# Kernel optimization log

Hardware: AMD Instinct MI355X
Metric: run time of the kernel (lower is better)

The kernel has to match this reference:

```python
import jax, jax.numpy as jnp
import numpy as np

HID = 4096; NH = 32; NKV = 8; HD = 128; EPS = 1e-6; BASE = 10000.0

def _rmsnorm(x, w):
    # RMSNorm over last (head_dim) axis
    return x * jax.lax.rsqrt(jnp.mean(x * x, axis=-1, keepdims=True) + EPS) * w

def _rope(x, positions):
    # neox-style rotary on (b, s, h, HD): rotate halves
    half = HD // 2
    inv_freq = 1.0 / (BASE ** (jnp.arange(0, HD, 2, dtype=jnp.float32) / HD))  # (half,)
    ang = positions.astype(jnp.float32)[:, None] * inv_freq                    # (s, half)
    cos = jnp.cos(ang)[None, :, None, :]
    sin = jnp.sin(ang)[None, :, None, :]
    x1, x2 = x[..., :half], x[..., half:]
    return jnp.concatenate([x1 * cos - x2 * sin, x2 * cos + x1 * sin], axis=-1)

def setup_inputs() -> dict:
    key = jax.random.key(0)
    k0, k1, k2 = jax.random.split(key, 3)
    b, s = 4, 1024
    return {
        "h_shard": jax.random.normal(k0, (b, s, HID), jnp.float32),
        "positions": jnp.arange(s, dtype=jnp.int32),
        "w_qkv": jax.random.normal(k1, (NH * HD + 2 * NKV * HD, HID), jnp.float32) * 0.02,
        "w_o": jax.random.normal(k2, (HID, NH * HD), jnp.float32) * 0.02,
        "q_norm_w": jnp.ones((HD,), jnp.float32),
        "k_norm_w": jnp.ones((HD,), jnp.float32),
    }

def reference(h_shard, positions, w_qkv, w_o, q_norm_w, k_norm_w):
    b, s, _ = h_shard.shape
    q_sz, kv_sz = NH * HD, NKV * HD
    # fused QKV projection (world_size=1 -> ag_mm is a plain matmul x @ W.T)
    qkv = h_shard @ w_qkv.T                                   # (b, s, q_sz + 2*kv_sz)
    q = qkv[..., :q_sz].reshape(b, s, NH, HD)
    k = qkv[..., q_sz:q_sz + kv_sz].reshape(b, s, NKV, HD)
    v = qkv[..., q_sz + kv_sz:].reshape(b, s, NKV, HD)
    # per-head RMSNorm then RoPE on q/k (Qwen3 ordering)
    q = _rope(_rmsnorm(q, q_norm_w), positions)
    k = _rope(_rmsnorm(k, k_norm_w), positions)
    # GQA SDPA without materializing repeated KV: group query heads per kv head
    g = NH // NKV
    qg = q.reshape(b, s, NKV, g, HD)
    scores = jnp.einsum('bskgd,btkd->bkgst', qg, k) / jnp.sqrt(jnp.float32(HD))
    causal = jnp.tril(jnp.ones((s, s), dtype=bool))
    scores = jnp.where(causal, scores, -jnp.inf)
    probs = jax.nn.softmax(scores, axis=-1)
    attn = jnp.einsum('bkgst,btkd->bskgd', probs, v).reshape(b, s, q_sz)
    # output projection (mm_rs -> plain matmul for world_size=1)
    return attn @ w_o.T
```

## Files before the change

### kernel.cpp

```cpp
#include <hip/hip_runtime.h>

typedef __bf16 bf16;
typedef __bf16 bf16x4 __attribute__((ext_vector_type(4)));
typedef __bf16 bf16x8 __attribute__((ext_vector_type(8)));
typedef float f32x4 __attribute__((ext_vector_type(4)));

#define HID 4096
#define QKV_N 6144
#define NTOK 4096

__device__ __forceinline__ void gload_lds16(const bf16* g, bf16* l) {
  __builtin_amdgcn_global_load_lds(
      (__attribute__((address_space(1))) void*)(g),
      (__attribute__((address_space(3))) void*)(l), 16, 0, 0);
}

__global__ void cvt_kernel(const float4* __restrict__ s, bf16x4* __restrict__ d) {
  int i = blockIdx.x * blockDim.x + threadIdx.x;
  float4 v = s[i];
  bf16x4 o;
  o[0] = (bf16)v.x; o[1] = (bf16)v.y; o[2] = (bf16)v.z; o[3] = (bf16)v.w;
  d[i] = o;
}

template <typename OutT>
__global__ __launch_bounds__(512, 2) void gemm_bt256(
    const bf16* __restrict__ A, const bf16* __restrict__ Bm,
    OutT* __restrict__ C, int M, int N, int K)
{
  __shared__ __align__(16) bf16 As[2][256 * 64];
  __shared__ __align__(16) bf16 Bs[2][256 * 64];

  const int tid = threadIdx.x;
  const int w = tid >> 6, l = tid & 63;
  const int quad = l >> 4, lane16 = l & 15;
  const int sw = lane16 & 7;
  const int lrow = l >> 3;
  const int lk = (l & 7) ^ lrow;

  const int nwg = gridDim.x * gridDim.y;
  int bid = blockIdx.y * gridDim.x + blockIdx.x;
  bid = (bid & 7) * (nwg >> 3) + (bid >> 3);
  const int row0 = (bid / gridDim.x) * 256;
  const int col0 = (bid % gridDim.x) * 256;

  const int wm = (w >> 2) * 128;
  const int wn = (w & 3) * 64;

  f32x4 acc[2][2][4][2];
#pragma unroll
  for (int mq = 0; mq < 2; ++mq)
#pragma unroll
    for (int nq = 0; nq < 2; ++nq)
#pragma unroll
      for (int im = 0; im < 4; ++im)
#pragma unroll
        for (int in_ = 0; in_ < 2; ++in_) acc[mq][nq][im][in_] = (f32x4){0.f, 0.f, 0.f, 0.f};

  bf16x8 af[4][2];
  bf16x8 bf0[2][2], bf1[2][2];

  auto stA = [&](int buf, int half, int kt) {
    const bf16* g = A + (size_t)(row0 + half * 128 + w * 8 + lrow) * K + kt * 64 + lk * 8;
    bf16* s = &As[buf][(half * 128 + w * 8) * 64 + l * 8];
    gload_lds16(g, s);
    gload_lds16(g + (size_t)64 * K, s + 64 * 64);
  };
  auto stB = [&](int buf, int half, int kt) {
    const bf16* g = Bm + (size_t)(col0 + half * 128 + w * 8 + lrow) * K + kt * 64 + lk * 8;
    bf16* s = &Bs[buf][(half * 128 + w * 8) * 64 + l * 8];
    gload_lds16(g, s);
    gload_lds16(g + (size_t)64 * K, s + 64 * 64);
  };

  auto loadA = [&](const bf16* Ap, int mq) {
#pragma unroll
    for (int im = 0; im < 4; ++im)
#pragma unroll
      for (int kk = 0; kk < 2; ++kk)
        af[im][kk] = *(const bf16x8*)&Ap[(wm + mq * 64 + im * 16 + lane16) * 64 +
                                         (((kk * 4 + quad) ^ sw) * 8)];
  };
  auto loadB = [&](const bf16* Bp, bf16x8 (&dst)[2][2], int nq) {
#pragma unroll
    for (int in_ = 0; in_ < 2; ++in_)
#pragma unroll
      for (int kk = 0; kk < 2; ++kk)
        dst[in_][kk] = *(const bf16x8*)&Bp[(wn + nq * 32 + in_ * 16 + lane16) * 64 +
                                           (((kk * 4 + quad) ^ sw) * 8)];
  };
  auto mma = [&](bf16x8 (&b)[2][2], f32x4 (&ac)[4][2]) {
#pragma unroll
    for (int im = 0; im < 4; ++im)
#pragma unroll
      for (int in_ = 0; in_ < 2; ++in_) {
        ac[im][in_] = __builtin_amdgcn_mfma_f32_16x16x32_bf16(af[im][0], b[in_][0], ac[im][in_], 0, 0, 0);
        ac[im][in_] = __builtin_amdgcn_mfma_f32_16x16x32_bf16(af[im][1], b[in_][1], ac[im][in_], 0, 0, 0);
      }
  };

  const int nt = K >> 6;

  stB(0, 0, 0); stB(0, 1, 0); stA(0, 0, 0); stA(0, 1, 0);
  stB(1, 0, 1); stB(1, 1, 1); stA(1, 0, 1);
  asm volatile("s_waitcnt vmcnt(6)" ::: "memory");
  __builtin_amdgcn_s_barrier();

  for (int t = 0; t < nt; ++t) {
    const int p = t & 1;
    const bf16* Ap = As[p];
    const bf16* Bp = Bs[p];

    loadA(Ap, 0);
    loadB(Bp, bf0, 0);
    if (t + 1 < nt) stA(p ^ 1, 1, t + 1);
    __builtin_amdgcn_sched_barrier(0);
    __builtin_amdgcn_s_barrier();
    asm volatile("s_waitcnt lgkmcnt(0)" ::: "memory");
    __builtin_amdgcn_sched_barrier(0);
    __builtin_amdgcn_s_setprio(1);
    mma(bf0, acc[0][0]);
    __builtin_amdgcn_s_setprio(0);
    __builtin_amdgcn_sched_barrier(0);
    __builtin_amdgcn_s_barrier();

    loadB(Bp, bf1, 1);
    __builtin_amdgcn_sched_barrier(0);
    __builtin_amdgcn_s_barrier();
    asm volatile("s_waitcnt lgkmcnt(0)" ::: "memory");
    __builtin_amdgcn_sched_barrier(0);
    __builtin_amdgcn_s_setprio(1);
    mma(bf1, acc[0][1]);
    __builtin_amdgcn_s_setprio(0);
    __builtin_amdgcn_sched_barrier(0);
    __builtin_amdgcn_s_barrier();

    loadA(Ap, 1);
    if (t + 2 < nt) { stB(p, 0, t + 2); stB(p, 1, t + 2); }
    __builtin_amdgcn_sched_barrier(0);
    __builtin_amdgcn_s_barrier();
    asm volatile("s_waitcnt lgkmcnt(0)" ::: "memory");
    __builtin_amdgcn_sched_barrier(0);
    __builtin_amdgcn_s_setprio(1);
    mma(bf1, acc[1][1]);
    __builtin_amdgcn_s_setprio(0);
    __builtin_amdgcn_sched_barrier(0);
    __builtin_amdgcn_s_barrier();

    if (t + 2 < nt) stA(p, 0, t + 2);
    __builtin_amdgcn_sched_barrier(0);
    __builtin_amdgcn_s_barrier();
    __builtin_amdgcn_s_setprio(1);
    mma(bf0, acc[1][0]);
    __builtin_amdgcn_s_setprio(0);
    __builtin_amdgcn_sched_barrier(0);
    if (t + 2 < nt) asm volatile("s_waitcnt vmcnt(6)" ::: "memory");
    else            asm volatile("s_waitcnt vmcnt(0)" ::: "memory");
    __builtin_amdgcn_s_barrier();
  }

#pragma unroll
  for (int mq = 0; mq < 2; ++mq)
#pragma unroll
    for (int im = 0; im < 4; ++im)
#pragma unroll
      for (int r = 0; r < 4; ++r) {
        int row = row0 + wm + mq * 64 + im * 16 + quad * 4 + r;
        OutT* cp = C + (size_t)row * N + col0 + wn;
#pragma unroll
        for (int nq = 0; nq < 2; ++nq)
#pragma unroll
          for (int in_ = 0; in_ < 2; ++in_)
            cp[nq * 32 + in_ * 16 + lane16] = (OutT)acc[mq][nq][im][in_][r];
      }
}

__global__ __launch_bounds__(256) void norm_rope_kernel(
    bf16* __restrict__ qkv, const int* __restrict__ pos,
    const float* __restrict__ qw, const float* __restrict__ kw)
{
  int g = blockIdx.x * 4 + (threadIdx.x >> 6);
  int tok = g / 40;
  int slot = g % 40;
  int d = threadIdx.x & 63;
  bf16* base;
  const float* w;
  if (slot < 32) { base = qkv + (size_t)tok * QKV_N + slot * 128; w = qw; }
  else           { base = qkv + (size_t)tok * QKV_N + HID + (slot - 32) * 128; w = kw; }
  float x1 = (float)base[d], x2 = (float)base[d + 64];
  float ss = x1 * x1 + x2 * x2;
#pragma unroll
  for (int m = 1; m < 64; m <<= 1) ss += __shfl_xor(ss, m, 64);
  float rn = rsqrtf(ss * (1.0f / 128.0f) + 1e-6f);
  x1 = x1 * rn * w[d];
  x2 = x2 * rn * w[d + 64];
  int p = pos[tok & 1023];
  float invf = exp2f(-0.20762050593045952f * (float)d);
  float ang = (float)p * invf;
  float sn, c;
  sincosf(ang, &sn, &c);
  base[d]      = (bf16)(x1 * c - x2 * sn);
  base[d + 64] = (bf16)(x2 * c + x1 * sn);
}

__global__ __launch_bounds__(256) void flash_kernel(
    const bf16* __restrict__ qkv, bf16* __restrict__ attn)
{
  __shared__ bf16 Ks[2][64 * 128];
  __shared__ bf16 Vt[2][128 * 64];
  __shared__ bf16 Ps[4][16 * 72];

  const int bh = blockIdx.y;
  const int qt = ((bh >> 4) & 1) ? (15 - blockIdx.x) : blockIdx.x;
  const int batch = bh >> 5;
  const int qh = bh & 31;
  const int kvh = qh >> 2;
  const int tid = threadIdx.x;
  const int w = tid >> 6, l = tid & 63;
  const int quad = l >> 4, lane16 = l & 15;
  const int sw = lane16 & 7;
  const size_t tok0 = (size_t)batch * 1024;
  const int q0 = qt * 64;

  bf16x8 qf[4];
  {
    const bf16* qrow = qkv + (tok0 + q0 + w * 16 + lane16) * QKV_N + qh * 128 + quad * 8;
#pragma unroll
    for (int kk = 0; kk < 4; ++kk) qf[kk] = *(const bf16x8*)(qrow + kk * 32);
  }

  f32x4 O[8];
#pragma unroll
  for (int id = 0; id < 8; ++id) O[id] = (f32x4){0.f, 0.f, 0.f, 0.f};
  float m_run[4], l_run[4];
#pragma unroll
  for (int r = 0; r < 4; ++r) { m_run[r] = -1e30f; l_run[r] = 0.f; }

  const float scale = 0.08838834764831845f;
  bf16x8 vreg[4];

  auto stage_K = [&](int j, int buf) {
#pragma unroll
    for (int r = 0; r < 4; ++r) {
      int i = r * 4 + w;
      int rloc = i * 4 + (l >> 4);
      int o = (l & 15) ^ (rloc & 7);
      const bf16* g = qkv + (tok0 + j * 64 + rloc) * QKV_N + HID + kvh * 128 + o * 8;
      gload_lds16(g, &Ks[buf][i * 512 + l * 8]);
    }
  };
  auto load_V = [&](int j) {
#pragma unroll
    for (int c = 0; c < 4; ++c) {
      int d0 = (c * 4 + w) * 8;
      vreg[c] = *(const bf16x8*)(qkv + (tok0 + j * 64 + l) * QKV_N + HID + 1024 + kvh * 128 + d0);
    }
  };
  auto write_V = [&](int buf) {
#pragma unroll
    for (int c = 0; c < 4; ++c) {
      int d0 = (c * 4 + w) * 8;
#pragma unroll
      for (int e = 0; e < 8; ++e) {
        int d = d0 + e;
        Vt[buf][d * 64 + (((l >> 3) ^ (d & 7)) * 8) + (l & 7)] = vreg[c][e];
      }
    }
  };

  stage_K(0, 0);
  load_V(0);
  write_V(0);
  __syncthreads();

  for (int j = 0; j <= qt; ++j) {
    const int p = j & 1;
    if (j < qt) { stage_K(j + 1, p ^ 1); load_V(j + 1); }

    f32x4 s[4];
#pragma unroll
    for (int in_ = 0; in_ < 4; ++in_) s[in_] = (f32x4){0.f, 0.f, 0.f, 0.f};
#pragma unroll
    for (int kk = 0; kk < 4; ++kk) {
#pragma unroll
      for (int in_ = 0; in_ < 4; ++in_) {
        bf16x8 b = *(const bf16x8*)&Ks[p][(in_ * 16 + lane16) * 128 + (((kk * 4 + quad) ^ sw) * 8)];
        s[in_] = __builtin_amdgcn_mfma_f32_16x16x32_bf16(qf[kk], b, s[in_], 0, 0, 0);
      }
    }

    if (j < qt) write_V(p ^ 1);

    const bool edge = (j == qt);
#pragma unroll
    for (int r = 0; r < 4; ++r) {
      float rm = -1e30f;
#pragma unroll
      for (int in_ = 0; in_ < 4; ++in_) {
        float v = s[in_][r] * scale;
        if (edge) {
          int t_abs = j * 64 + in_ * 16 + lane16;
          int q_abs = q0 + w * 16 + quad * 4 + r;
          v = (t_abs <= q_abs) ? v : -1e30f;
        }
        s[in_][r] = v;
        rm = fmaxf(rm, v);
      }
#pragma unroll
      for (int m = 1; m < 16; m <<= 1) rm = fmaxf(rm, __shfl_xor(rm, m, 64));
      float mn = fmaxf(m_run[r], rm);
      float alpha = __expf(m_run[r] - mn);
      m_run[r] = mn;
      float rs = 0.f;
#pragma unroll
      for (int in_ = 0; in_ < 4; ++in_) {
        float pv = __expf(s[in_][r] - mn);
        s[in_][r] = pv;
        rs += pv;
      }
#pragma unroll
      for (int m = 1; m < 16; m <<= 1) rs += __shfl_xor(rs, m, 64);
      l_run[r] = l_run[r] * alpha + rs;
#pragma unroll
      for (int id = 0; id < 8; ++id) O[id][r] *= alpha;
#pragma unroll
      for (int in_ = 0; in_ < 4; ++in_)
        Ps[w][(quad * 4 + r) * 72 + in_ * 16 + lane16] = (bf16)s[in_][r];
    }

#pragma unroll
    for (int kt = 0; kt < 2; ++kt) {
      bf16x8 a = *(const bf16x8*)&Ps[w][lane16 * 72 + kt * 32 + quad * 8];
#pragma unroll
      for (int id = 0; id < 8; ++id) {
        bf16x8 b = *(const bf16x8*)&Vt[p][(id * 16 + lane16) * 64 + (((kt * 4 + quad) ^ sw) * 8)];
        O[id] = __builtin_amdgcn_mfma_f32_16x16x32_bf16(a, b, O[id], 0, 0, 0);
      }
    }
    __syncthreads();
  }

#pragma unroll
  for (int r = 0; r < 4; ++r) {
    float inv = 1.0f / l_run[r];
    int row = q0 + w * 16 + quad * 4 + r;
    bf16* orow = attn + (tok0 + row) * (size_t)HID + qh * 128;
#pragma unroll
    for (int id = 0; id < 8; ++id) orow[id * 16 + lane16] = (bf16)(O[id][r] * inv);
  }
}

extern "C" void kernel_launch(void* const* d_in, const int* in_sizes, int n_in,
                              void* d_out, int out_size, void* d_ws, size_t ws_size,
                              hipStream_t stream) {
  const float* h    = (const float*)d_in[0];
  const int*   pos  = (const int*)d_in[1];
  const float* wqkv = (const float*)d_in[2];
  const float* wo   = (const float*)d_in[3];
  const float* qw   = (const float*)d_in[4];
  const float* kw   = (const float*)d_in[5];
  float* out = (float*)d_out;

  bf16* hb    = (bf16*)d_ws;
  bf16* wqkvb = hb + 16777216;
  bf16* wob   = wqkvb + 25165824;
  bf16* qkvb  = wob + 16777216;
  bf16* attnb = qkvb + 25165824;

  cvt_kernel<<<16384, 256, 0, stream>>>((const float4*)h, (bf16x4*)hb);
  cvt_kernel<<<24576, 256, 0, stream>>>((const float4*)wqkv, (bf16x4*)wqkvb);
  cvt_kernel<<<16384, 256, 0, stream>>>((const float4*)wo, (bf16x4*)wob);

  gemm_bt256<bf16><<<dim3(24, 16), 512, 0, stream>>>(hb, wqkvb, qkvb, NTOK, QKV_N, HID);

  norm_rope_kernel<<<NTOK * 40 / 4, 256, 0, stream>>>(qkvb, pos, qw, kw);

  flash_kernel<<<dim3(16, 128), 256, 0, stream>>>(qkvb, attnb);

  gemm_bt256<float><<<dim3(16, 16), 512, 0, stream>>>(attnb, wob, out, NTOK, HID, HID);
}
```

Baseline: 787.4 us.

## Double-buffer A fragments and prefetch next tile's A during GEMM main loop

Restructures the bf16 GEMM main loop so A register fragments are double-buffered (aF0/aF1). The next k-tile's first A fragment loads right after the global-to-LDS wait, overlapping with the last MFMA phase. Both B fragment sets load up front, the explicit lgkmcnt waits are removed, and the stage-ahead schedule now prefetches a full A tile (both halves) with a vmcnt(4) wait. This cuts LDS-read stalls before each MFMA phase, at the cost of more VGPRs and dropping the explicit lgkmcnt synchronisation, so the compiler's own waits must keep it correct.

```diff
diff --git a/kernel.cpp b/kernel.cpp
--- a/kernel.cpp
+++ b/kernel.cpp
@@ -8,6 +8,9 @@
 #define HID 4096
 #define QKV_N 6144
 #define NTOK 4096
+
+#define SB()  __builtin_amdgcn_sched_barrier(0)
+#define BAR() __builtin_amdgcn_s_barrier()
 
 __device__ __forceinline__ void gload_lds16(const bf16* g, bf16* l) {
   __builtin_amdgcn_global_load_lds(
@@ -57,8 +60,8 @@
 #pragma unroll
         for (int in_ = 0; in_ < 2; ++in_) acc[mq][nq][im][in_] = (f32x4){0.f, 0.f, 0.f, 0.f};
 
-  bf16x8 af[4][2];
-  bf16x8 bf0[2][2], bf1[2][2];
+  bf16x8 aF0[4][2], aF1[4][2];
+  bf16x8 bF0[2][2], bF1[2][2];
 
   auto stA = [&](int buf, int half, int kt) {
     const bf16* g = A + (size_t)(row0 + half * 128 + w * 8 + lrow) * K + kt * 64 + lk * 8;
@@ -73,13 +76,13 @@
     gload_lds16(g + (size_t)64 * K, s + 64 * 64);
   };
 
-  auto loadA = [&](const bf16* Ap, int mq) {
+  auto loadA = [&](const bf16* Ap, bf16x8 (&dst)[4][2], int mq) {
 #pragma unroll
     for (int im = 0; im < 4; ++im)
 #pragma unroll
       for (int kk = 0; kk < 2; ++kk)
-        af[im][kk] = *(const bf16x8*)&Ap[(wm + mq * 64 + im * 16 + lane16) * 64 +
-                                         (((kk * 4 + quad) ^ sw) * 8)];
+        dst[im][kk] = *(const bf16x8*)&Ap[(wm + mq * 64 + im * 16 + lane16) * 64 +
+                                          (((kk * 4 + quad) ^ sw) * 8)];
   };
   auto loadB = [&](const bf16* Bp, bf16x8 (&dst)[2][2], int nq) {
 #pragma unroll
@@ -89,74 +92,66 @@
         dst[in_][kk] = *(const bf16x8*)&Bp[(wn + nq * 32 + in_ * 16 + lane16) * 64 +
                                            (((kk * 4 + quad) ^ sw) * 8)];
   };
-  auto mma = [&](bf16x8 (&b)[2][2], f32x4 (&ac)[4][2]) {
+  auto mma = [&](bf16x8 (&a)[4][2], bf16x8 (&b)[2][2], f32x4 (&ac)[4][2]) {
 #pragma unroll
     for (int im = 0; im < 4; ++im)
 #pragma unroll
       for (int in_ = 0; in_ < 2; ++in_) {
-        ac[im][in_] = __builtin_amdgcn_mfma_f32_16x16x32_bf16(af[im][0], b[in_][0], ac[im][in_], 0, 0, 0);
-        ac[im][in_] = __builtin_amdgcn_mfma_f32_16x16x32_bf16(af[im][1], b[in_][1], ac[im][in_], 0, 0, 0);
+        ac[im][in_] = __builtin_amdgcn_mfma_f32_16x16x32_bf16(a[im][0], b[in_][0], ac[im][in_], 0, 0, 0);
+        ac[im][in_] = __builtin_amdgcn_mfma_f32_16x16x32_bf16(a[im][1], b[in_][1], ac[im][in_], 0, 0, 0);
       }
   };
 
   const int nt = K >> 6;
 
   stB(0, 0, 0); stB(0, 1, 0); stA(0, 0, 0); stA(0, 1, 0);
-  stB(1, 0, 1); stB(1, 1, 1); stA(1, 0, 1);
-  asm volatile("s_waitcnt vmcnt(6)" ::: "memory");
-  __builtin_amdgcn_s_barrier();
+  if (nt > 1) {
+    stB(1, 0, 1); stB(1, 1, 1); stA(1, 0, 1); stA(1, 1, 1);
+    asm volatile("s_waitcnt vmcnt(8)" ::: "memory");
+  } else {
+    asm volatile("s_waitcnt vmcnt(0)" ::: "memory");
+  }
+  BAR();
+  SB();
+  loadA(As[0], aF0, 0);
 
   for (int t = 0; t < nt; ++t) {
     const int p = t & 1;
     const bf16* Ap = As[p];
     const bf16* Bp = Bs[p];
 
-    loadA(Ap, 0);
-    loadB(Bp, bf0, 0);
-    if (t + 1 < nt) stA(p ^ 1, 1, t + 1);
-    __builtin_amdgcn_sched_barrier(0);
-    __builtin_amdgcn_s_barrier();
-    asm volatile("s_waitcnt lgkmcnt(0)" ::: "memory");
-    __builtin_amdgcn_sched_barrier(0);
+    loadB(Bp, bF0, 0);
+    loadB(Bp, bF1, 1);
+    SB(); BAR(); SB();
     __builtin_amdgcn_s_setprio(1);
-    mma(bf0, acc[0][0]);
+    mma(aF0, bF0, acc[0][0]);
     __builtin_amdgcn_s_setprio(0);
-    __builtin_amdgcn_sched_barrier(0);
-    __builtin_amdgcn_s_barrier();
-
-    loadB(Bp, bf1, 1);
-    __builtin_amdgcn_sched_barrier(0);
-    __builtin_amdgcn_s_barrier();
-    asm volatile("s_waitcnt lgkmcnt(0)" ::: "memory");
-    __builtin_amdgcn_sched_barrier(0);
+    SB(); BAR(); SB();
+
+    loadA(Ap, aF1, 1);
+    SB(); BAR(); SB();
     __builtin_amdgcn_s_setprio(1);
-    mma(bf1, acc[0][1]);
+    mma(aF0, bF1, acc[0][1]);
     __builtin_amdgcn_s_setprio(0);
-    __builtin_amdgcn_sched_barrier(0);
-    __builtin_amdgcn_s_barrier();
-
-    loadA(Ap, 1);
+    SB(); BAR(); SB();
+
     if (t + 2 < nt) { stB(p, 0, t + 2); stB(p, 1, t + 2); }
-    __builtin_amdgcn_sched_barrier(0);
-    __builtin_amdgcn_s_barrier();
-    asm volatile("s_waitcnt lgkmcnt(0)" ::: "memory");
-    __builtin_amdgcn_sched_barrier(0);
+    SB(); BAR(); SB();
     __builtin_amdgcn_s_setprio(1);
-    mma(bf1, acc[1][1]);
+    mma(aF1, bF1, acc[1][1]);
     __builtin_amdgcn_s_setprio(0);
-    __builtin_amdgcn_sched_barrier(0);
-    __builtin_amdgcn_s_barrier();
-
-    if (t + 2 < nt) stA(p, 0, t + 2);
-    __builtin_amdgcn_sched_barrier(0);
-    __builtin_amdgcn_s_barrier();
+    SB();
+    if (t + 2 < nt) asm volatile("s_waitcnt vmcnt(4)" ::: "memory");
+    else            asm volatile("s_waitcnt vmcnt(0)" ::: "memory");
+    BAR(); SB();
+
+    if (t + 1 < nt) loadA(As[p ^ 1], aF0, 0);
+    if (t + 2 < nt) { stA(p, 0, t + 2); stA(p, 1, t + 2); }
+    SB(); BAR(); SB();
     __builtin_amdgcn_s_setprio(1);
-    mma(bf0, acc[1][0]);
+    mma(aF1, bF0, acc[1][0]);
     __builtin_amdgcn_s_setprio(0);
-    __builtin_amdgcn_sched_barrier(0);
-    if (t + 2 < nt) asm volatile("s_waitcnt vmcnt(6)" ::: "memory");
-    else            asm volatile("s_waitcnt vmcnt(0)" ::: "memory");
-    __builtin_amdgcn_s_barrier();
+    SB(); BAR(); SB();
   }
 
 #pragma unroll
```

Result: slower. 804.8 us (+2.2%).
